# Optimization experiments

Measured on AMD Instinct MI355X. Metric: run time of the kernel, lower is better.

The kernel has to match this reference:

```python
import jax, jax.numpy as jnp
import numpy as np

N_HEADS = 16
D_MODEL = 1024
D_K = 64
D_V = 64
LN_EPS = 1e-6


def setup_inputs() -> dict:
    key = jax.random.key(0)
    ks = jax.random.split(key, 16)
    B, L, D = 4, 512, D_MODEL
    s = 1.0 / np.sqrt(D)
    return {
        "q": jax.random.normal(ks[0], (B, L, D), jnp.float32),
        "k": jax.random.normal(ks[1], (B, L, D), jnp.float32),
        "v": jax.random.normal(ks[2], (B, L, D), jnp.float32),
        "bias": jax.random.normal(ks[3], (B, N_HEADS, L, L), jnp.float32),
        "graph_attn_bias": jax.random.normal(ks[4], (B, N_HEADS, L, L), jnp.float32),
        # projection weights stored as [in, out] (math-equivalent to torch Linear)
        "wq": jax.random.normal(ks[5], (D, N_HEADS * D_K), jnp.float32) * s,
        "bq": jnp.zeros((N_HEADS * D_K,), jnp.float32),
        "wk": jax.random.normal(ks[6], (D, N_HEADS * D_K), jnp.float32) * s,
        "bk": jnp.zeros((N_HEADS * D_K,), jnp.float32),
        "wv": jax.random.normal(ks[7], (D, N_HEADS * D_V), jnp.float32) * s,
        "bv": jnp.zeros((N_HEADS * D_V,), jnp.float32),
        "wo": jax.random.normal(ks[8], (N_HEADS * D_V, D), jnp.float32) * s,
        "bo": jnp.zeros((D,), jnp.float32),
        "ln_g": jnp.ones((D,), jnp.float32),
        "ln_b": jnp.zeros((D,), jnp.float32),
    }


def reference(q, k, v, bias, graph_attn_bias, wq, bq, wk, bk, wv, bv, wo, bo, ln_g, ln_b):
    B, Lq, D = q.shape
    H, dk, dv = N_HEADS, D_K, D_V
    residual = q
    # fused QKV projections, split heads -> [B, H, L, d]
    qh = (q @ wq + bq).reshape(B, Lq, H, dk).transpose(0, 2, 1, 3)
    kh = (k @ wk + bk).reshape(B, k.shape[1], H, dk).transpose(0, 2, 1, 3)
    vh = (v @ wv + bv).reshape(B, v.shape[1], H, dv).transpose(0, 2, 1, 3)
    # graph scaled dot-product attention: scores + mask bias + structural bias
    scores = jnp.einsum("bhqd,bhkd->bhqk", qh / np.sqrt(dk).astype(qh.dtype), kh)
    scores = scores + bias + graph_attn_bias
    weights = jax.nn.softmax(scores, axis=-1)
    ctx = jnp.einsum("bhqk,bhkd->bhqd", weights, vh)  # [B,H,Lq,dv]
    ctx = ctx.transpose(0, 2, 1, 3).reshape(B, Lq, H * dv)
    out = ctx @ wo + bo + residual
    # LayerNorm(eps=1e-6)
    mu = jnp.mean(out, axis=-1, keepdims=True)
    var = jnp.var(out, axis=-1, keepdims=True)
    out = (out - mu) * jax.lax.rsqrt(var + LN_EPS) * ln_g + ln_b
    return out
```

## Files before the change

kernel.cpp:

```cpp
#include <hip/hip_runtime.h>

#define D_MODEL 1024
#define N_HEADS 16
#define DK 64
#define LSEQ 512
#define BATCH 4
#define M_ROWS (BATCH * LSEQ)

typedef unsigned short ushort_t;
typedef __attribute__((ext_vector_type(8))) short short8;
typedef __attribute__((ext_vector_type(4))) float floatx4;

__device__ __forceinline__ float bf2f(unsigned short u) {
    return __uint_as_float(((unsigned int)u) << 16);
}
__device__ __forceinline__ unsigned short f2bf(float f) {
    unsigned int u = __float_as_uint(f);
    u += 0x7fffu + ((u >> 16) & 1u);
    return (unsigned short)(u >> 16);
}

__global__ __launch_bounds__(256) void cast3_kernel(
    const float* __restrict__ a, const float* __restrict__ b,
    const float* __restrict__ c, ushort_t* __restrict__ oa,
    ushort_t* __restrict__ ob, ushort_t* __restrict__ oc, int n)
{
    const float* src = (blockIdx.y == 0) ? a : (blockIdx.y == 1) ? b : c;
    ushort_t* dst = (blockIdx.y == 0) ? oa : (blockIdx.y == 1) ? ob : oc;
    int i = (blockIdx.x * 256 + threadIdx.x) * 4;
    if (i + 3 < n) {
        float4 v = *(const float4*)(src + i);
        ushort4 o = make_ushort4(f2bf(v.x), f2bf(v.y), f2bf(v.z), f2bf(v.w));
        *(ushort4*)(dst + i) = o;
    }
}

__global__ __launch_bounds__(256) void transpose4_kernel(
    const float* __restrict__ w0, const float* __restrict__ w1,
    const float* __restrict__ w2, const float* __restrict__ w3,
    ushort_t* __restrict__ o0, ushort_t* __restrict__ o1,
    ushort_t* __restrict__ o2, ushort_t* __restrict__ o3)
{
    __shared__ float tile[32][33];
    const float* W = (blockIdx.z == 0) ? w0 : (blockIdx.z == 1) ? w1
                   : (blockIdx.z == 2) ? w2 : w3;
    ushort_t* O = (blockIdx.z == 0) ? o0 : (blockIdx.z == 1) ? o1
                : (blockIdx.z == 2) ? o2 : o3;
    const int tx = threadIdx.x & 31;
    const int ty = threadIdx.x >> 5;
    const int kbase = blockIdx.y * 32;
    const int nbase = blockIdx.x * 32;
    #pragma unroll
    for (int j = 0; j < 4; ++j)
        tile[ty + 8 * j][tx] = W[(size_t)(kbase + ty + 8 * j) * 1024 + nbase + tx];
    __syncthreads();
    #pragma unroll
    for (int j = 0; j < 4; ++j) {
        int n = nbase + ty + 8 * j;
        O[(size_t)n * 1024 + kbase + tx] = f2bf(tile[tx][ty + 8 * j]);
    }
}

template <bool OUT_BF16, bool ADD_BVEC, bool ADD_RES, bool OUT_VT>
__device__ __forceinline__ void gemm_bt_body(
    const ushort_t* __restrict__ A, const ushort_t* __restrict__ Bt,
    const float* __restrict__ bvec, const float* __restrict__ res,
    void* __restrict__ outp, int N, int K, int kStart, int kEnd,
    int rowBase, int colBase, ushort_t* As, ushort_t* Bs)
{
    const int tid = threadIdx.x;
    const int l = tid & 63;
    const int w = tid >> 6;
    const int wave_m = w >> 1;
    const int wave_n = w & 1;

    const int srow8 = l >> 3;
    const int cgl = ((l & 7) + srow8) & 7;
    const ushort_t* gA0 = A  + (size_t)(rowBase + w * 16 + 0 + srow8) * K + cgl * 8;
    const ushort_t* gA1 = A  + (size_t)(rowBase + w * 16 + 8 + srow8) * K + cgl * 8;
    const ushort_t* gB0 = Bt + (size_t)(colBase + w * 16 + 0 + srow8) * K + cgl * 8;
    const ushort_t* gB1 = Bt + (size_t)(colBase + w * 16 + 8 + srow8) * K + cgl * 8;
    ushort_t* lA0 = As + w * 1024;
    ushort_t* lA1 = As + w * 1024 + 512;
    ushort_t* lB0 = Bs + w * 1024;
    ushort_t* lB1 = Bs + w * 1024 + 512;

    floatx4 acc[2][2];
    #pragma unroll
    for (int i = 0; i < 2; ++i)
        #pragma unroll
        for (int j = 0; j < 2; ++j)
            acc[i][j] = (floatx4){0.f, 0.f, 0.f, 0.f};

    const int fm = l & 15;
    const int fg = l >> 4;

    for (int k0 = kStart; k0 < kEnd; k0 += 64) {
        __builtin_amdgcn_global_load_lds(
            (const __attribute__((address_space(1))) void*)(gA0 + k0),
            (__attribute__((address_space(3))) void*)lA0, 16, 0, 0);
        __builtin_amdgcn_global_load_lds(
            (const __attribute__((address_space(1))) void*)(gA1 + k0),
            (__attribute__((address_space(3))) void*)lA1, 16, 0, 0);
        __builtin_amdgcn_global_load_lds(
            (const __attribute__((address_space(1))) void*)(gB0 + k0),
            (__attribute__((address_space(3))) void*)lB0, 16, 0, 0);
        __builtin_amdgcn_global_load_lds(
            (const __attribute__((address_space(1))) void*)(gB1 + k0),
            (__attribute__((address_space(3))) void*)lB1, 16, 0, 0);
        __syncthreads();

        short8 afrag[2][2], bfrag[2][2];
        #pragma unroll
        for (int mi = 0; mi < 2; ++mi)
            #pragma unroll
            for (int kt = 0; kt < 2; ++kt) {
                int p = ((kt * 4 + fg) - fm) & 7;
                afrag[mi][kt] = *(const short8*)
                    &As[(wave_m * 32 + mi * 16 + fm) * 64 + p * 8];
            }
        #pragma unroll
        for (int ni = 0; ni < 2; ++ni)
            #pragma unroll
            for (int kt = 0; kt < 2; ++kt) {
                int p = ((kt * 4 + fg) - fm) & 7;
                bfrag[ni][kt] = *(const short8*)
                    &Bs[(wave_n * 32 + ni * 16 + fm) * 64 + p * 8];
            }

        #pragma unroll
        for (int kt = 0; kt < 2; ++kt)
            #pragma unroll
            for (int mi = 0; mi < 2; ++mi)
                #pragma unroll
                for (int ni = 0; ni < 2; ++ni)
                    acc[mi][ni] = __builtin_amdgcn_mfma_f32_16x16x32_bf16(
                        afrag[mi][kt], bfrag[ni][kt], acc[mi][ni], 0, 0, 0);
        __syncthreads();
    }

    const int crow0 = rowBase + wave_m * 32 + fg * 4;
    const int ccol0 = colBase + wave_n * 32 + fm;
    #pragma unroll
    for (int mi = 0; mi < 2; ++mi) {
        #pragma unroll
        for (int ni = 0; ni < 2; ++ni) {
            const int col = ccol0 + ni * 16;
            const float bb = ADD_BVEC ? bvec[col] : 0.f;
            if (OUT_VT) {
                const int row0 = crow0 + mi * 16;
                ushort4 pk;
                pk.x = f2bf(acc[mi][ni][0] + bb);
                pk.y = f2bf(acc[mi][ni][1] + bb);
                pk.z = f2bf(acc[mi][ni][2] + bb);
                pk.w = f2bf(acc[mi][ni][3] + bb);
                const size_t base =
                    ((size_t)((row0 >> 9) * 16 + (col >> 6)) * 64 + (col & 63)) * 512;
                *(ushort4*)&((ushort_t*)outp)[base + (row0 & 511)] = pk;
            } else {
                #pragma unroll
                for (int r = 0; r < 4; ++r) {
                    const int row = crow0 + mi * 16 + r;
                    float v = acc[mi][ni][r] + bb;
                    if (ADD_RES) v += res[(size_t)row * N + col];
                    if (OUT_BF16)
                        ((ushort_t*)outp)[(size_t)row * N + col] = f2bf(v);
                    else
                        ((float*)outp)[(size_t)row * N + col] = v;
                }
            }
        }
    }
}

__global__ __launch_bounds__(256) void gemm_qkv(
    const ushort_t* a0, const ushort_t* a1, const ushort_t* a2,
    const ushort_t* t0, const ushort_t* t1, const ushort_t* t2,
    const float* b0, const float* b1, const float* b2,
    ushort_t* o0, ushort_t* o1, ushort_t* o2)
{
    __shared__ ushort_t As[64 * 64];
    __shared__ ushort_t Bs[64 * 64];
    const int z = blockIdx.z;
    if (z == 2) {
        gemm_bt_body<true, true, false, true>(a2, t2, b2, nullptr, o2, D_MODEL,
                                              D_MODEL, 0, D_MODEL,
                                              blockIdx.y * 64, blockIdx.x * 64, As, Bs);
    } else {
        const ushort_t* A  = (z == 0) ? a0 : a1;
        const ushort_t* Bt = (z == 0) ? t0 : t1;
        const float* bv    = (z == 0) ? b0 : b1;
        ushort_t* o        = (z == 0) ? o0 : o1;
        gemm_bt_body<true, true, false, false>(A, Bt, bv, nullptr, o, D_MODEL,
                                               D_MODEL, 0, D_MODEL,
                                               blockIdx.y * 64, blockIdx.x * 64, As, Bs);
    }
}

__global__ __launch_bounds__(256) void gemm_out(
    const ushort_t* __restrict__ A, const ushort_t* __restrict__ Bt,
    const float* __restrict__ bvec, const float* __restrict__ res,
    float* __restrict__ out0, float* __restrict__ out1)
{
    __shared__ ushort_t As[64 * 64];
    __shared__ ushort_t Bs[64 * 64];
    if (blockIdx.z == 0)
        gemm_bt_body<false, true, true, false>(A, Bt, bvec, res, out0, D_MODEL,
                                               D_MODEL, 0, 512,
                                               blockIdx.y * 64, blockIdx.x * 64, As, Bs);
    else
        gemm_bt_body<false, false, false, false>(A, Bt, nullptr, nullptr, out1, D_MODEL,
                                                 D_MODEL, 512, 1024,
                                                 blockIdx.y * 64, blockIdx.x * 64, As, Bs);
}

#define P_STRIDE 520

__global__ __launch_bounds__(256, 4) void attn_mfma(
    const ushort_t* __restrict__ qh, const ushort_t* __restrict__ kh,
    const ushort_t* __restrict__ vt, const float* __restrict__ bias,
    const float* __restrict__ gbias, ushort_t* __restrict__ ctx)
{
    __shared__ __attribute__((aligned(16))) ushort_t Qs[16 * 72];
    __shared__ __attribute__((aligned(16))) ushort_t P[16 * P_STRIDE];
    __shared__ float redm[4][16];
    __shared__ float reds[4][16];

    const int tid = threadIdx.x;
    const int l = tid & 63;
    const int w = tid >> 6;
    const int m = l & 15;
    const int g = l >> 4;

    const int bh = blockIdx.y;
    const int h = bh & (N_HEADS - 1);
    const int b = bh >> 4;
    const int q0 = blockIdx.x * 16;

    const ushort_t* Qg = qh + ((size_t)(b * LSEQ + q0)) * D_MODEL + h * DK;
    const ushort_t* Kg = kh + ((size_t)(b * LSEQ)) * D_MODEL + h * DK;
    const ushort_t* Vt_g = vt + (size_t)bh * DK * LSEQ;

    if (tid < 128) {
        int row = tid >> 3, seg = tid & 7;
        short8 t = *(const short8*)(Qg + (size_t)row * D_MODEL + seg * 8);
        *(short8*)&Qs[row * 72 + seg * 8] = t;
    }
    __syncthreads();

    short8 aq0 = *(const short8*)&Qs[m * 72 + g * 8];
    short8 aq1 = *(const short8*)&Qs[m * 72 + g * 8 + 32];

    floatx4 acc[8];
    #pragma unroll 2
    for (int it = 0; it < 8; ++it) {
        const int kb = it * 64 + w * 16;
        const ushort_t* kr = Kg + (size_t)(kb + m) * D_MODEL + g * 8;
        short8 bk0 = *(const short8*)kr;
        short8 bk1 = *(const short8*)(kr + 32);
        floatx4 a = (floatx4){0.f, 0.f, 0.f, 0.f};
        a = __builtin_amdgcn_mfma_f32_16x16x32_bf16(aq0, bk0, a, 0, 0, 0);
        a = __builtin_amdgcn_mfma_f32_16x16x32_bf16(aq1, bk1, a, 0, 0, 0);
        acc[it] = a;
    }

    const float* bp = bias  + ((size_t)bh * LSEQ + q0) * LSEQ + w * 16 + m;
    const float* gp = gbias + ((size_t)bh * LSEQ + q0) * LSEQ + w * 16 + m;
    float bsum[8][4];
    #pragma unroll
    for (int it = 0; it < 8; ++it)
        #pragma unroll
        for (int r = 0; r < 4; ++r) {
            const size_t off = (size_t)(g * 4 + r) * LSEQ + it * 64;
            bsum[it][r] = bp[off] + gp[off];
        }
    #pragma unroll
    for (int it = 0; it < 8; ++it)
        #pragma unroll
        for (int r = 0; r < 4; ++r)
            acc[it][r] = acc[it][r] * 0.125f + bsum[it][r];

    float mx[4];
    #pragma unroll
    for (int r = 0; r < 4; ++r) {
        float pm = fmaxf(
            fmaxf(fmaxf(acc[0][r], acc[1][r]), fmaxf(acc[2][r], acc[3][r])),
            fmaxf(fmaxf(acc[4][r], acc[5][r]), fmaxf(acc[6][r], acc[7][r])));
        #pragma unroll
        for (int d = 1; d < 16; d <<= 1)
            pm = fmaxf(pm, __shfl_xor(pm, d, 64));
        mx[r] = pm;
    }
    if (m == 0) {
        #pragma unroll
        for (int r = 0; r < 4; ++r) redm[w][g * 4 + r] = mx[r];
    }
    __syncthreads();
    #pragma unroll
    for (int r = 0; r < 4; ++r)
        mx[r] = fmaxf(fmaxf(redm[0][g * 4 + r], redm[1][g * 4 + r]),
                      fmaxf(redm[2][g * 4 + r], redm[3][g * 4 + r]));

    float sm[4] = {0.f, 0.f, 0.f, 0.f};
    #pragma unroll
    for (int it = 0; it < 8; ++it)
        #pragma unroll
        for (int r = 0; r < 4; ++r) {
            float e = __expf(acc[it][r] - mx[r]);
            sm[r] += e;
            P[(g * 4 + r) * P_STRIDE + it * 64 + w * 16 + m] = f2bf(e);
        }
    #pragma unroll
    for (int r = 0; r < 4; ++r) {
        #pragma unroll
        for (int d = 1; d < 16; d <<= 1)
            sm[r] += __shfl_xor(sm[r], d, 64);
    }
    if (m == 0) {
        #pragma unroll
        for (int r = 0; r < 4; ++r) reds[w][g * 4 + r] = sm[r];
    }
    __syncthreads();
    float rinv[4];
    #pragma unroll
    for (int r = 0; r < 4; ++r)
        rinv[r] = 1.0f / (reds[0][g * 4 + r] + reds[1][g * 4 + r] +
                          reds[2][g * 4 + r] + reds[3][g * 4 + r]);

    floatx4 oacc = (floatx4){0.f, 0.f, 0.f, 0.f};
    const ushort_t* vrow = Vt_g + (size_t)(w * 16 + m) * LSEQ + g * 8;
    const ushort_t* prow = &P[(size_t)m * P_STRIDE + g * 8];
    #pragma unroll 2
    for (int vtile = 0; vtile < 8; ++vtile) {
        #pragma unroll
        for (int kt = 0; kt < 2; ++kt) {
            const int ko = vtile * 64 + kt * 32;
            short8 pf = *(const short8*)(prow + ko);
            short8 vf = *(const short8*)(vrow + ko);
            oacc = __builtin_amdgcn_mfma_f32_16x16x32_bf16(pf, vf, oacc, 0, 0, 0);
        }
    }

    {
        const int qrow0 = g * 4;
        const int dcol = w * 16 + m;
        ushort_t* cp = ctx + ((size_t)(b * LSEQ + q0 + qrow0)) * D_MODEL + h * DK + dcol;
        #pragma unroll
        for (int r = 0; r < 4; ++r)
            cp[(size_t)r * D_MODEL] = f2bf(oacc[r] * rinv[r]);
    }
}

__global__ __launch_bounds__(256) void ln_kernel(
    float* __restrict__ x, const float* __restrict__ part2,
    const float* __restrict__ g, const float* __restrict__ beta)
{
    const int row = blockIdx.x;
    float* xr = x + (size_t)row * D_MODEL;
    const float* pr = part2 + (size_t)row * D_MODEL;
    const int tid = threadIdx.x;

    float v[4];
    float s = 0.f, sq = 0.f;
    #pragma unroll
    for (int j = 0; j < 4; ++j) {
        v[j] = xr[tid + 256 * j] + pr[tid + 256 * j];
        s += v[j];
        sq += v[j] * v[j];
    }
    __shared__ float rs[256], rq[256];
    rs[tid] = s;
    rq[tid] = sq;
    __syncthreads();
    for (int st = 128; st > 0; st >>= 1) {
        if (tid < st) { rs[tid] += rs[tid + st]; rq[tid] += rq[tid + st]; }
        __syncthreads();
    }
    const float mean = rs[0] * (1.0f / D_MODEL);
    const float var = rq[0] * (1.0f / D_MODEL) - mean * mean;
    const float rinv = rsqrtf(var + 1e-6f);
    #pragma unroll
    for (int j = 0; j < 4; ++j) {
        int n = tid + 256 * j;
        xr[n] = (v[j] - mean) * rinv * g[n] + beta[n];
    }
}

extern "C" void kernel_launch(void* const* d_in, const int* in_sizes, int n_in,
                              void* d_out, int out_size, void* d_ws, size_t ws_size,
                              hipStream_t stream)
{
    const float* q     = (const float*)d_in[0];
    const float* k     = (const float*)d_in[1];
    const float* v     = (const float*)d_in[2];
    const float* bias  = (const float*)d_in[3];
    const float* gbias = (const float*)d_in[4];
    const float* wq    = (const float*)d_in[5];
    const float* bq    = (const float*)d_in[6];
    const float* wk    = (const float*)d_in[7];
    const float* bk    = (const float*)d_in[8];
    const float* wv    = (const float*)d_in[9];
    const float* bv    = (const float*)d_in[10];
    const float* wo    = (const float*)d_in[11];
    const float* bo    = (const float*)d_in[12];
    const float* ln_g  = (const float*)d_in[13];
    const float* ln_b  = (const float*)d_in[14];

    const size_t MB = 1u << 20;
    char* wsb = (char*)d_ws;
    ushort_t* vb   = (ushort_t*)(wsb + 0 * MB);
    ushort_t* wqb  = (ushort_t*)(wsb + 4 * MB);
    ushort_t* wkb  = (ushort_t*)(wsb + 6 * MB);
    ushort_t* wvb  = (ushort_t*)(wsb + 8 * MB);
    ushort_t* wob  = (ushort_t*)(wsb + 10 * MB);
    ushort_t* qhb  = (ushort_t*)(wsb + 12 * MB);
    ushort_t* khb  = (ushort_t*)(wsb + 16 * MB);
    ushort_t* vtb  = (ushort_t*)(wsb + 20 * MB);
    ushort_t* ctxb = (ushort_t*)(wsb + 24 * MB);
    float* out1 = (float*)(wsb + 12 * MB);
    ushort_t* qb = (ushort_t*)d_out;
    ushort_t* kb = (ushort_t*)d_out + (size_t)M_ROWS * D_MODEL;
    float* outp = (float*)d_out;

    const int NELEM = M_ROWS * D_MODEL;

    cast3_kernel<<<dim3(NELEM / 1024, 3), 256, 0, stream>>>(
        q, k, v, qb, kb, vb, NELEM);
    transpose4_kernel<<<dim3(32, 32, 4), 256, 0, stream>>>(
        wq, wk, wv, wo, wqb, wkb, wvb, wob);

    dim3 gqkv(D_MODEL / 64, M_ROWS / 64, 3);
    gemm_qkv<<<gqkv, 256, 0, stream>>>(
        qb, kb, vb, wqb, wkb, wvb, bq, bk, bv, qhb, khb, vtb);

    dim3 ablk(LSEQ / 16, BATCH * N_HEADS);
    attn_mfma<<<ablk, 256, 0, stream>>>(qhb, khb, vtb, bias, gbias, ctxb);

    dim3 gout(D_MODEL / 64, M_ROWS / 64, 2);
    gemm_out<<<gout, 256, 0, stream>>>(ctxb, wob, bo, q, outp, out1);

    ln_kernel<<<M_ROWS, 256, 0, stream>>>(outp, out1, ln_g, ln_b);
}
```

Measured before the change: 266.7 us.

## Process two 16-row query tiles per attention block to reuse K and V loads

Each attention block now handles 32 query rows as two 16-row sub-tiles, so every K and V fragment loaded from global memory feeds two MFMA streams. This halves the redundant K/V reads across blocks and halves the grid size. In exchange, register pressure and LDS use roughly double, so occupancy is lowered via launch bounds, and fewer blocks may underfill the GPU.

Result: no change. 271.9 us (+2.0%).

```diff
diff --git a/kernel.cpp b/kernel.cpp
--- a/kernel.cpp
+++ b/kernel.cpp
@@ -216,15 +216,16 @@
 
 #define P_STRIDE 520
 
-__global__ __launch_bounds__(256, 4) void attn_mfma(
+__global__ __launch_bounds__(256, 3) void attn_mfma(
     const ushort_t* __restrict__ qh, const ushort_t* __restrict__ kh,
     const ushort_t* __restrict__ vt, const float* __restrict__ bias,
     const float* __restrict__ gbias, ushort_t* __restrict__ ctx)
 {
-    __shared__ __attribute__((aligned(16))) ushort_t Qs[16 * 72];
-    __shared__ __attribute__((aligned(16))) ushort_t P[16 * P_STRIDE];
-    __shared__ float redm[4][16];
-    __shared__ float reds[4][16];
+    __shared__ __attribute__((aligned(16))) ushort_t Qs[32 * 72];
+    __shared__ __attribute__((aligned(16))) ushort_t PA[16 * P_STRIDE];
+    __shared__ __attribute__((aligned(16))) ushort_t PB[16 * P_STRIDE];
+    __shared__ float redmA[4][16], redsA[4][16];
+    __shared__ float redmB[4][16], redsB[4][16];
 
     const int tid = threadIdx.x;
     const int l = tid & 63;
@@ -235,119 +236,160 @@
     const int bh = blockIdx.y;
     const int h = bh & (N_HEADS - 1);
     const int b = bh >> 4;
-    const int q0 = blockIdx.x * 16;
+    const int q0 = blockIdx.x * 32;
 
     const ushort_t* Qg = qh + ((size_t)(b * LSEQ + q0)) * D_MODEL + h * DK;
     const ushort_t* Kg = kh + ((size_t)(b * LSEQ)) * D_MODEL + h * DK;
     const ushort_t* Vt_g = vt + (size_t)bh * DK * LSEQ;
 
-    if (tid < 128) {
+    {
         int row = tid >> 3, seg = tid & 7;
         short8 t = *(const short8*)(Qg + (size_t)row * D_MODEL + seg * 8);
         *(short8*)&Qs[row * 72 + seg * 8] = t;
     }
     __syncthreads();
 
-    short8 aq0 = *(const short8*)&Qs[m * 72 + g * 8];
-    short8 aq1 = *(const short8*)&Qs[m * 72 + g * 8 + 32];
-
-    floatx4 acc[8];
-    #pragma unroll 2
+    short8 aqA0 = *(const short8*)&Qs[m * 72 + g * 8];
+    short8 aqA1 = *(const short8*)&Qs[m * 72 + g * 8 + 32];
+    short8 aqB0 = *(const short8*)&Qs[(16 + m) * 72 + g * 8];
+    short8 aqB1 = *(const short8*)&Qs[(16 + m) * 72 + g * 8 + 32];
+
+    floatx4 accA[8], accB[8];
+    #pragma unroll
     for (int it = 0; it < 8; ++it) {
         const int kb = it * 64 + w * 16;
         const ushort_t* kr = Kg + (size_t)(kb + m) * D_MODEL + g * 8;
         short8 bk0 = *(const short8*)kr;
         short8 bk1 = *(const short8*)(kr + 32);
         floatx4 a = (floatx4){0.f, 0.f, 0.f, 0.f};
-        a = __builtin_amdgcn_mfma_f32_16x16x32_bf16(aq0, bk0, a, 0, 0, 0);
-        a = __builtin_amdgcn_mfma_f32_16x16x32_bf16(aq1, bk1, a, 0, 0, 0);
-        acc[it] = a;
-    }
-
-    const float* bp = bias  + ((size_t)bh * LSEQ + q0) * LSEQ + w * 16 + m;
-    const float* gp = gbias + ((size_t)bh * LSEQ + q0) * LSEQ + w * 16 + m;
-    float bsum[8][4];
+        a = __builtin_amdgcn_mfma_f32_16x16x32_bf16(aqA0, bk0, a, 0, 0, 0);
+        a = __builtin_amdgcn_mfma_f32_16x16x32_bf16(aqA1, bk1, a, 0, 0, 0);
+        accA[it] = a;
+        floatx4 bacc = (floatx4){0.f, 0.f, 0.f, 0.f};
+        bacc = __builtin_amdgcn_mfma_f32_16x16x32_bf16(aqB0, bk0, bacc, 0, 0, 0);
+        bacc = __builtin_amdgcn_mfma_f32_16x16x32_bf16(aqB1, bk1, bacc, 0, 0, 0);
+        accB[it] = bacc;
+    }
+
+    const float* bpA = bias  + ((size_t)bh * LSEQ + q0) * LSEQ + w * 16 + m;
+    const float* gpA = gbias + ((size_t)bh * LSEQ + q0) * LSEQ + w * 16 + m;
+    const float* bpB = bpA + 16 * LSEQ;
+    const float* gpB = gpA + 16 * LSEQ;
+    #pragma unroll
+    for (int it = 0; it < 8; ++it) {
+        float bA[4], bB[4];
+        #pragma unroll
+        for (int r = 0; r < 4; ++r) {
+            const size_t off = (size_t)(g * 4 + r) * LSEQ + it * 64;
+            bA[r] = bpA[off] + gpA[off];
+            bB[r] = bpB[off] + gpB[off];
+        }
+        #pragma unroll
+        for (int r = 0; r < 4; ++r) {
+            accA[it][r] = accA[it][r] * 0.125f + bA[r];
+            accB[it][r] = accB[it][r] * 0.125f + bB[r];
+        }
+    }
+
+    float mxA[4], mxB[4];
+    #pragma unroll
+    for (int r = 0; r < 4; ++r) {
+        float pa = fmaxf(
+            fmaxf(fmaxf(accA[0][r], accA[1][r]), fmaxf(accA[2][r], accA[3][r])),
+            fmaxf(fmaxf(accA[4][r], accA[5][r]), fmaxf(accA[6][r], accA[7][r])));
+        float pb = fmaxf(
+            fmaxf(fmaxf(accB[0][r], accB[1][r]), fmaxf(accB[2][r], accB[3][r])),
+            fmaxf(fmaxf(accB[4][r], accB[5][r]), fmaxf(accB[6][r], accB[7][r])));
+        #pragma unroll
+        for (int d = 1; d < 16; d <<= 1) {
+            pa = fmaxf(pa, __shfl_xor(pa, d, 64));
+            pb = fmaxf(pb, __shfl_xor(pb, d, 64));
+        }
+        mxA[r] = pa;
+        mxB[r] = pb;
+    }
+    if (m == 0) {
+        #pragma unroll
+        for (int r = 0; r < 4; ++r) {
+            redmA[w][g * 4 + r] = mxA[r];
+            redmB[w][g * 4 + r] = mxB[r];
+        }
+    }
+    __syncthreads();
+    #pragma unroll
+    for (int r = 0; r < 4; ++r) {
+        mxA[r] = fmaxf(fmaxf(redmA[0][g * 4 + r], redmA[1][g * 4 + r]),
+                       fmaxf(redmA[2][g * 4 + r], redmA[3][g * 4 + r]));
+        mxB[r] = fmaxf(fmaxf(redmB[0][g * 4 + r], redmB[1][g * 4 + r]),
+                       fmaxf(redmB[2][g * 4 + r], redmB[3][g * 4 + r]));
+    }
+
+    float smA[4] = {0.f, 0.f, 0.f, 0.f};
+    float smB[4] = {0.f, 0.f, 0.f, 0.f};
     #pragma unroll
     for (int it = 0; it < 8; ++it)
         #pragma unroll
         for (int r = 0; r < 4; ++r) {
-            const size_t off = (size_t)(g * 4 + r) * LSEQ + it * 64;
-            bsum[it][r] = bp[off] + gp[off];
-        }
-    #pragma unroll
-    for (int it = 0; it < 8; ++it)
-        #pragma unroll
-        for (int r = 0; r < 4; ++r)
-            acc[it][r] = acc[it][r] * 0.125f + bsum[it][r];
-
-    float mx[4];
+            float eA = __expf(accA[it][r] - mxA[r]);
+            float eB = __expf(accB[it][r] - mxB[r]);
+            smA[r] += eA;
+            smB[r] += eB;
+            PA[(g * 4 + r) * P_STRIDE + it * 64 + w * 16 + m] = f2bf(eA);
+            PB[(g * 4 + r) * P_STRIDE + it * 64 + w * 16 + m] = f2bf(eB);
+        }
     #pragma unroll
     for (int r = 0; r < 4; ++r) {
-        float pm = fmaxf(
-            fmaxf(fmaxf(acc[0][r], acc[1][r]), fmaxf(acc[2][r], acc[3][r])),
-            fmaxf(fmaxf(acc[4][r], acc[5][r]), fmaxf(acc[6][r], acc[7][r])));
-        #pragma unroll
-        for (int d = 1; d < 16; d <<= 1)
-            pm = fmaxf(pm, __shfl_xor(pm, d, 64));
-        mx[r] = pm;
+        #pragma unroll
+        for (int d = 1; d < 16; d <<= 1) {
+            smA[r] += __shfl_xor(smA[r], d, 64);
+            smB[r] += __shfl_xor(smB[r], d, 64);
+        }
     }
     if (m == 0) {
         #pragma unroll
-        for (int r = 0; r < 4; ++r) redm[w][g * 4 + r] = mx[r];
+        for (int r = 0; r < 4; ++r) {
+            redsA[w][g * 4 + r] = smA[r];
+            redsB[w][g * 4 + r] = smB[r];
+        }
     }
     __syncthreads();
-    #pragma unroll
-    for (int r = 0; r < 4; ++r)
-        mx[r] = fmaxf(fmaxf(redm[0][g * 4 + r], redm[1][g * 4 + r]),
-                      fmaxf(redm[2][g * 4 + r], redm[3][g * 4 + r]));
-
-    float sm[4] = {0.f, 0.f, 0.f, 0.f};
-    #pragma unroll
-    for (int it = 0; it < 8; ++it)
-        #pragma unroll
-        for (int r = 0; r < 4; ++r) {
-            float e = __expf(acc[it][r] - mx[r]);
-            sm[r] += e;
-            P[(g * 4 + r) * P_STRIDE + it * 64 + w * 16 + m] = f2bf(e);
-        }
+    float rinvA[4], rinvB[4];
     #pragma unroll
     for (int r = 0; r < 4; ++r) {
-        #pragma unroll
-        for (int d = 1; d < 16; d <<= 1)
-            sm[r] += __shfl_xor(sm[r], d, 64);
-    }
-    if (m == 0) {
-        #pragma unroll
-        for (int r = 0; r < 4; ++r) reds[w][g * 4 + r] = sm[r];
-    }
-    __syncthreads();
-    float rinv[4];
-    #pragma unroll
-    for (int r = 0; r < 4; ++r)
-        rinv[r] = 1.0f / (reds[0][g * 4 + r] + reds[1][g * 4 + r] +
-                          reds[2][g * 4 + r] + reds[3][g * 4 + r]);
-
-    floatx4 oacc = (floatx4){0.f, 0.f, 0.f, 0.f};
+        rinvA[r] = 1.0f / (redsA[0][g * 4 + r] + redsA[1][g * 4 + r] +
+                           redsA[2][g * 4 + r] + redsA[3][g * 4 + r]);
+        rinvB[r] = 1.0f / (redsB[0][g * 4 + r] + redsB[1][g * 4 + r] +
+                           redsB[2][g * 4 + r] + redsB[3][g * 4 + r]);
+    }
+
+    floatx4 oaccA = (floatx4){0.f, 0.f, 0.f, 0.f};
+    floatx4 oaccB = (floatx4){0.f, 0.f, 0.f, 0.f};
     const ushort_t* vrow = Vt_g + (size_t)(w * 16 + m) * LSEQ + g * 8;
-    const ushort_t* prow = &P[(size_t)m * P_STRIDE + g * 8];
-    #pragma unroll 2
+    const ushort_t* prowA = &PA[(size_t)m * P_STRIDE + g * 8];
+    const ushort_t* prowB = &PB[(size_t)m * P_STRIDE + g * 8];
+    #pragma unroll
     for (int vtile = 0; vtile < 8; ++vtile) {
         #pragma unroll
         for (int kt = 0; kt < 2; ++kt) {
             const int ko = vtile * 64 + kt * 32;
-            short8 pf = *(const short8*)(prow + ko);
             short8 vf = *(const short8*)(vrow + ko);
-            oacc = __builtin_amdgcn_mfma_f32_16x16x32_bf16(pf, vf, oacc, 0, 0, 0);
+            short8 pfA = *(const short8*)(prowA + ko);
+            short8 pfB = *(const short8*)(prowB + ko);
+            oaccA = __builtin_amdgcn_mfma_f32_16x16x32_bf16(pfA, vf, oaccA, 0, 0, 0);
+            oaccB = __builtin_amdgcn_mfma_f32_16x16x32_bf16(pfB, vf, oaccB, 0, 0, 0);
         }
     }
 
     {
         const int qrow0 = g * 4;
         const int dcol = w * 16 + m;
-        ushort_t* cp = ctx + ((size_t)(b * LSEQ + q0 + qrow0)) * D_MODEL + h * DK + dcol;
-        #pragma unroll
-        for (int r = 0; r < 4; ++r)
-            cp[(size_t)r * D_MODEL] = f2bf(oacc[r] * rinv[r]);
+        ushort_t* cpA = ctx + ((size_t)(b * LSEQ + q0 + qrow0)) * D_MODEL + h * DK + dcol;
+        ushort_t* cpB = cpA + (size_t)16 * D_MODEL;
+        #pragma unroll
+        for (int r = 0; r < 4; ++r) {
+            cpA[(size_t)r * D_MODEL] = f2bf(oaccA[r] * rinvA[r]);
+            cpB[(size_t)r * D_MODEL] = f2bf(oaccB[r] * rinvB[r]);
+        }
     }
 }
 
@@ -433,7 +475,7 @@
     gemm_qkv<<<gqkv, 256, 0, stream>>>(
         qb, kb, vb, wqb, wkb, wvb, bq, bk, bv, qhb, khb, vtb);
 
-    dim3 ablk(LSEQ / 16, BATCH * N_HEADS);
+    dim3 ablk(LSEQ / 32, BATCH * N_HEADS);
     attn_mfma<<<ablk, 256, 0, stream>>>(qhb, khb, vtb, bias, gbias, ctxb);
 
     dim3 gout(D_MODEL / 64, M_ROWS / 64, 2);
```

## Split attention into score-softmax kernel and PV kernel with global P buffer

Applied to the files above, without the earlier changes.

Splits the fused attention kernel into two. The first computes scaled QK scores for 32 query rows into shared memory, adds both biases with coalesced float4 row loads, runs the softmax per row and writes normalized bf16 probabilities to a global buffer. The second kernel reads P and V^T to compute the context with MFMA. The aim is coalesced, vectorized reads of the large bias tensors, in place of the strided scalar loads used before. The cost is an extra 32 MB round trip for P, an additional launch, and a 64-float register array per thread that may lower occupancy.

New measurement: 293.1 us. 1.1x slower.

```diff
diff --git a/kernel.cpp b/kernel.cpp
--- a/kernel.cpp
+++ b/kernel.cpp
@@ -214,17 +214,15 @@
                                                  blockIdx.y * 64, blockIdx.x * 64, As, Bs);
 }
 
-#define P_STRIDE 520
-
-__global__ __launch_bounds__(256, 4) void attn_mfma(
+#define S_STRIDE 516
+
+__global__ __launch_bounds__(256, 2) void attn_qks(
     const ushort_t* __restrict__ qh, const ushort_t* __restrict__ kh,
-    const ushort_t* __restrict__ vt, const float* __restrict__ bias,
-    const float* __restrict__ gbias, ushort_t* __restrict__ ctx)
-{
-    __shared__ __attribute__((aligned(16))) ushort_t Qs[16 * 72];
-    __shared__ __attribute__((aligned(16))) ushort_t P[16 * P_STRIDE];
-    __shared__ float redm[4][16];
-    __shared__ float reds[4][16];
+    const float* __restrict__ bias, const float* __restrict__ gbias,
+    ushort_t* __restrict__ Pg)
+{
+    __shared__ __attribute__((aligned(16))) float S[32 * S_STRIDE];
+    __shared__ __attribute__((aligned(16))) ushort_t Qs[32 * 72];
 
     const int tid = threadIdx.x;
     const int l = tid & 63;
@@ -235,119 +233,128 @@
     const int bh = blockIdx.y;
     const int h = bh & (N_HEADS - 1);
     const int b = bh >> 4;
-    const int q0 = blockIdx.x * 16;
+    const int q0 = blockIdx.x * 32;
 
     const ushort_t* Qg = qh + ((size_t)(b * LSEQ + q0)) * D_MODEL + h * DK;
     const ushort_t* Kg = kh + ((size_t)(b * LSEQ)) * D_MODEL + h * DK;
-    const ushort_t* Vt_g = vt + (size_t)bh * DK * LSEQ;
-
-    if (tid < 128) {
+
+    {
         int row = tid >> 3, seg = tid & 7;
         short8 t = *(const short8*)(Qg + (size_t)row * D_MODEL + seg * 8);
         *(short8*)&Qs[row * 72 + seg * 8] = t;
     }
     __syncthreads();
 
-    short8 aq0 = *(const short8*)&Qs[m * 72 + g * 8];
-    short8 aq1 = *(const short8*)&Qs[m * 72 + g * 8 + 32];
-
-    floatx4 acc[8];
-    #pragma unroll 2
+    short8 aqA0 = *(const short8*)&Qs[m * 72 + g * 8];
+    short8 aqA1 = *(const short8*)&Qs[m * 72 + g * 8 + 32];
+    short8 aqB0 = *(const short8*)&Qs[(16 + m) * 72 + g * 8];
+    short8 aqB1 = *(const short8*)&Qs[(16 + m) * 72 + g * 8 + 32];
+
+    #pragma unroll
     for (int it = 0; it < 8; ++it) {
         const int kb = it * 64 + w * 16;
         const ushort_t* kr = Kg + (size_t)(kb + m) * D_MODEL + g * 8;
         short8 bk0 = *(const short8*)kr;
         short8 bk1 = *(const short8*)(kr + 32);
         floatx4 a = (floatx4){0.f, 0.f, 0.f, 0.f};
-        a = __builtin_amdgcn_mfma_f32_16x16x32_bf16(aq0, bk0, a, 0, 0, 0);
-        a = __builtin_amdgcn_mfma_f32_16x16x32_bf16(aq1, bk1, a, 0, 0, 0);
-        acc[it] = a;
-    }
-
-    const float* bp = bias  + ((size_t)bh * LSEQ + q0) * LSEQ + w * 16 + m;
-    const float* gp = gbias + ((size_t)bh * LSEQ + q0) * LSEQ + w * 16 + m;
-    float bsum[8][4];
-    #pragma unroll
-    for (int it = 0; it < 8; ++it)
+        a = __builtin_amdgcn_mfma_f32_16x16x32_bf16(aqA0, bk0, a, 0, 0, 0);
+        a = __builtin_amdgcn_mfma_f32_16x16x32_bf16(aqA1, bk1, a, 0, 0, 0);
+        floatx4 bb = (floatx4){0.f, 0.f, 0.f, 0.f};
+        bb = __builtin_amdgcn_mfma_f32_16x16x32_bf16(aqB0, bk0, bb, 0, 0, 0);
+        bb = __builtin_amdgcn_mfma_f32_16x16x32_bf16(aqB1, bk1, bb, 0, 0, 0);
+        const int col = it * 64 + w * 16 + m;
         #pragma unroll
         for (int r = 0; r < 4; ++r) {
-            const size_t off = (size_t)(g * 4 + r) * LSEQ + it * 64;
-            bsum[it][r] = bp[off] + gp[off];
+            S[(g * 4 + r) * S_STRIDE + col] = a[r] * 0.125f;
+            S[(16 + g * 4 + r) * S_STRIDE + col] = bb[r] * 0.125f;
         }
-    #pragma unroll
-    for (int it = 0; it < 8; ++it)
-        #pragma unroll
-        for (int r = 0; r < 4; ++r)
-            acc[it][r] = acc[it][r] * 0.125f + bsum[it][r];
-
-    float mx[4];
+    }
+    __syncthreads();
+
+    const int row = tid >> 3;
+    const int s8 = tid & 7;
+    const size_t rbase = ((size_t)bh * LSEQ + q0 + row) * LSEQ + s8 * 64;
+    const float* bp = bias + rbase;
+    const float* gp = gbias + rbase;
+    const float* sp = &S[row * S_STRIDE + s8 * 64];
+
+    float v[64];
+    float mx = -1e30f;
+    #pragma unroll
+    for (int j = 0; j < 16; ++j) {
+        float4 b4 = *(const float4*)(bp + j * 4);
+        float4 g4 = *(const float4*)(gp + j * 4);
+        float4 s4 = *(const float4*)(sp + j * 4);
+        v[4 * j + 0] = s4.x + b4.x + g4.x;
+        v[4 * j + 1] = s4.y + b4.y + g4.y;
+        v[4 * j + 2] = s4.z + b4.z + g4.z;
+        v[4 * j + 3] = s4.w + b4.w + g4.w;
+        mx = fmaxf(mx, fmaxf(fmaxf(v[4 * j], v[4 * j + 1]),
+                             fmaxf(v[4 * j + 2], v[4 * j + 3])));
+    }
+    #pragma unroll
+    for (int d = 1; d < 8; d <<= 1) mx = fmaxf(mx, __shfl_xor(mx, d, 64));
+
+    float sm = 0.f;
+    #pragma unroll
+    for (int j = 0; j < 64; ++j) {
+        v[j] = __expf(v[j] - mx);
+        sm += v[j];
+    }
+    #pragma unroll
+    for (int d = 1; d < 8; d <<= 1) sm += __shfl_xor(sm, d, 64);
+    const float rinv = 1.0f / sm;
+
+    ushort_t* prow = Pg + rbase;
+    #pragma unroll
+    for (int j = 0; j < 8; ++j) {
+        short8 pk;
+        #pragma unroll
+        for (int e = 0; e < 8; ++e)
+            pk[e] = (short)f2bf(v[j * 8 + e] * rinv);
+        *(short8*)(prow + j * 8) = pk;
+    }
+}
+
+__global__ __launch_bounds__(256) void attn_pv(
+    const ushort_t* __restrict__ Pg, const ushort_t* __restrict__ vt,
+    ushort_t* __restrict__ ctx)
+{
+    const int tid = threadIdx.x;
+    const int l = tid & 63;
+    const int w = tid >> 6;
+    const int m = l & 15;
+    const int g = l >> 4;
+
+    const int bh = blockIdx.y;
+    const int h = bh & (N_HEADS - 1);
+    const int b = bh >> 4;
+    const int q0 = blockIdx.x * 32;
+
+    const ushort_t* Pb = Pg + ((size_t)bh * LSEQ + q0) * LSEQ;
+    const ushort_t* Vt_g = vt + (size_t)bh * DK * LSEQ;
+
+    floatx4 o0 = (floatx4){0.f, 0.f, 0.f, 0.f};
+    floatx4 o1 = (floatx4){0.f, 0.f, 0.f, 0.f};
+    const ushort_t* vrow = Vt_g + (size_t)(w * 16 + m) * LSEQ + g * 8;
+    const ushort_t* p0 = Pb + (size_t)m * LSEQ + g * 8;
+    const ushort_t* p1 = Pb + (size_t)(16 + m) * LSEQ + g * 8;
+
+    #pragma unroll
+    for (int ks = 0; ks < 16; ++ks) {
+        const int ko = ks * 32;
+        short8 vf = *(const short8*)(vrow + ko);
+        short8 pa = *(const short8*)(p0 + ko);
+        short8 pb = *(const short8*)(p1 + ko);
+        o0 = __builtin_amdgcn_mfma_f32_16x16x32_bf16(pa, vf, o0, 0, 0, 0);
+        o1 = __builtin_amdgcn_mfma_f32_16x16x32_bf16(pb, vf, o1, 0, 0, 0);
+    }
+
+    ushort_t* cp = ctx + ((size_t)(b * LSEQ + q0 + g * 4)) * D_MODEL + h * DK + w * 16 + m;
     #pragma unroll
     for (int r = 0; r < 4; ++r) {
-        float pm = fmaxf(
-            fmaxf(fmaxf(acc[0][r], acc[1][r]), fmaxf(acc[2][r], acc[3][r])),
-            fmaxf(fmaxf(acc[4][r], acc[5][r]), fmaxf(acc[6][r], acc[7][r])));
-        #pragma unroll
-        for (int d = 1; d < 16; d <<= 1)
-            pm = fmaxf(pm, __shfl_xor(pm, d, 64));
-        mx[r] = pm;
-    }
-    if (m == 0) {
-        #pragma unroll
-        for (int r = 0; r < 4; ++r) redm[w][g * 4 + r] = mx[r];
-    }
-    __syncthreads();
-    #pragma unroll
-    for (int r = 0; r < 4; ++r)
-        mx[r] = fmaxf(fmaxf(redm[0][g * 4 + r], redm[1][g * 4 + r]),
-                      fmaxf(redm[2][g * 4 + r], redm[3][g * 4 + r]));
-
-    float sm[4] = {0.f, 0.f, 0.f, 0.f};
-    #pragma unroll
-    for (int it = 0; it < 8; ++it)
-        #pragma unroll
-        for (int r = 0; r < 4; ++r) {
-            float e = __expf(acc[it][r] - mx[r]);
-            sm[r] += e;
-            P[(g * 4 + r) * P_STRIDE + it * 64 + w * 16 + m] = f2bf(e);
-        }
-    #pragma unroll
-    for (int r = 0; r < 4; ++r) {
-        #pragma unroll
-        for (int d = 1; d < 16; d <<= 1)
-            sm[r] += __shfl_xor(sm[r], d, 64);
-    }
-    if (m == 0) {
-        #pragma unroll
-        for (int r = 0; r < 4; ++r) reds[w][g * 4 + r] = sm[r];
-    }
-    __syncthreads();
-    float rinv[4];
-    #pragma unroll
-    for (int r = 0; r < 4; ++r)
-        rinv[r] = 1.0f / (reds[0][g * 4 + r] + reds[1][g * 4 + r] +
-                          reds[2][g * 4 + r] + reds[3][g * 4 + r]);
-
-    floatx4 oacc = (floatx4){0.f, 0.f, 0.f, 0.f};
-    const ushort_t* vrow = Vt_g + (size_t)(w * 16 + m) * LSEQ + g * 8;
-    const ushort_t* prow = &P[(size_t)m * P_STRIDE + g * 8];
-    #pragma unroll 2
-    for (int vtile = 0; vtile < 8; ++vtile) {
-        #pragma unroll
-        for (int kt = 0; kt < 2; ++kt) {
-            const int ko = vtile * 64 + kt * 32;
-            short8 pf = *(const short8*)(prow + ko);
-            short8 vf = *(const short8*)(vrow + ko);
-            oacc = __builtin_amdgcn_mfma_f32_16x16x32_bf16(pf, vf, oacc, 0, 0, 0);
-        }
-    }
-
-    {
-        const int qrow0 = g * 4;
-        const int dcol = w * 16 + m;
-        ushort_t* cp = ctx + ((size_t)(b * LSEQ + q0 + qrow0)) * D_MODEL + h * DK + dcol;
-        #pragma unroll
-        for (int r = 0; r < 4; ++r)
-            cp[(size_t)r * D_MODEL] = f2bf(oacc[r] * rinv[r]);
+        cp[(size_t)r * D_MODEL] = f2bf(o0[r]);
+        cp[(size_t)(16 + r) * D_MODEL] = f2bf(o1[r]);
     }
 }
 
@@ -417,6 +424,7 @@
     ushort_t* khb  = (ushort_t*)(wsb + 16 * MB);
     ushort_t* vtb  = (ushort_t*)(wsb + 20 * MB);
     ushort_t* ctxb = (ushort_t*)(wsb + 24 * MB);
+    ushort_t* pbuf = (ushort_t*)(wsb + 28 * MB);
     float* out1 = (float*)(wsb + 12 * MB);
     ushort_t* qb = (ushort_t*)d_out;
     ushort_t* kb = (ushort_t*)d_out + (size_t)M_ROWS * D_MODEL;
@@ -433,8 +441,9 @@
     gemm_qkv<<<gqkv, 256, 0, stream>>>(
         qb, kb, vb, wqb, wkb, wvb, bq, bk, bv, qhb, khb, vtb);
 
-    dim3 ablk(LSEQ / 16, BATCH * N_HEADS);
-    attn_mfma<<<ablk, 256, 0, stream>>>(qhb, khb, vtb, bias, gbias, ctxb);
+    dim3 ablk(LSEQ / 32, BATCH * N_HEADS);
+    attn_qks<<<ablk, 256, 0, stream>>>(qhb, khb, bias, gbias, pbuf);
+    attn_pv<<<ablk, 256, 0, stream>>>(pbuf, vtb, ctxb);
 
     dim3 gout(D_MODEL / 64, M_ROWS / 64, 2);
     gemm_out<<<gout, 256, 0, stream>>>(ctxb, wob, bo, q, outp, out1);
```
